# Kernel tuning notes

Measured on AMD Instinct MI355X. Metric: run time of the kernel, lower is better.

Reference implementation:

```python
import jax, jax.numpy as jnp
import numpy as np

H = 3        # num heads
K_ = 16      # codebook size per head (k_**H == k == 4096)
D = 768      # full vector dim
DH = D // H  # per-head dim


def setup_inputs() -> dict:
    key = jax.random.key(0)
    kx, kk, ka = jax.random.split(key, 3)
    x = jax.random.normal(kx, (16, 4096, D), dtype=jnp.float32)
    kernel = jax.random.normal(kk, (H, K_, DH), dtype=jnp.float32)
    alpha = jax.random.uniform(ka, (), dtype=jnp.float32)
    return {"x": x, "kernel": kernel, "alpha": alpha}


def reference(x, kernel, alpha):
    B, S, _ = x.shape
    xh = x.reshape(B, S, H, DH)  # split into per-head chunks
    # squared L2 distance [B,S,H,K_]; argmin identical to argmin of tf.norm
    sq = (jnp.sum(xh * xh, axis=-1)[..., None]
          - 2.0 * jnp.einsum('bshd,hkd->bshk', xh, kernel)
          + jnp.sum(kernel * kernel, axis=-1))
    ind = jnp.argmin(sq, axis=-1)              # [B,S,H] int
    v = kernel[jnp.arange(H), ind]             # per-head gather -> [B,S,H,DH]
    v = v.reshape(B, S, D)
    out = alpha * x + (1.0 - alpha) * v        # convex blend
    base = (K_ ** jnp.arange(H)).astype(ind.dtype)  # [1, K_, K_^2]
    code = jnp.sum(ind * base, axis=-1)        # packed code [B,S]
    return out, code
```

## Files before the change

### kernel.cpp

```cpp
#include <hip/hip_runtime.h>


#define NH 3
#define NK 16
#define DHEAD 256
#define DFULL 768
#define TB 4

typedef float f2 __attribute__((ext_vector_type(2)));

__device__ __forceinline__ float dpp_xor1(float x) {
    return __builtin_bit_cast(float, __builtin_amdgcn_mov_dpp(
        __builtin_bit_cast(int, x), 0xB1, 0xF, 0xF, false));
}
__device__ __forceinline__ float dpp_xor2(float x) {
    return __builtin_bit_cast(float, __builtin_amdgcn_mov_dpp(
        __builtin_bit_cast(int, x), 0x4E, 0xF, 0xF, false));
}
__device__ __forceinline__ float swz_xor4(float x) {
    return __builtin_bit_cast(float, __builtin_amdgcn_ds_swizzle(
        __builtin_bit_cast(int, x), 0x101F));
}
__device__ __forceinline__ float swz_xor8(float x) {
    return __builtin_bit_cast(float, __builtin_amdgcn_ds_swizzle(
        __builtin_bit_cast(int, x), 0x201F));
}
__device__ __forceinline__ float swz_xor16(float x) {
    return __builtin_bit_cast(float, __builtin_amdgcn_ds_swizzle(
        __builtin_bit_cast(int, x), 0x401F));
}

__global__ __launch_bounds__(256, 4) void rvq_head_kernel(
    const float* __restrict__ x,
    const float* __restrict__ cb,
    const float* __restrict__ alphap,
    float* __restrict__ out,
    float* __restrict__ codef,
    int tok_per_block)
{
    const int h = blockIdx.y;
    __shared__ float lc[NK * DHEAD];
    __shared__ float lps[NK * 16];
    __shared__ float lcn[NK];

    const int tid = threadIdx.x;

    const float4* cb4 = (const float4*)(cb + (size_t)h * NK * DHEAD);
    float4* lc4w = (float4*)lc;
    #pragma unroll
    for (int i = 0; i < 4; ++i) lc4w[tid + i * 256] = cb4[tid + i * 256];

    {
        const int r = tid >> 4, dd = (tid & 15) * 16;
        const float4* p = (const float4*)(cb + (size_t)h * NK * DHEAD + r * DHEAD + dd);
        float s = 0.f;
        #pragma unroll
        for (int q = 0; q < 4; ++q) {
            float4 c = p[q];
            s += c.x * c.x + c.y * c.y + c.z * c.z + c.w * c.w;
        }
        lps[tid] = s;
    }
    __syncthreads();
    if (tid < NK) {
        float s = 0.f;
        #pragma unroll
        for (int q = 0; q < 16; ++q) s += lps[tid * 16 + q];
        lcn[tid] = s;
    }
    __syncthreads();

    const int lane = tid & 63;
    const int wid  = tid >> 6;
    const int hl = (((lane >> 1) & 1) << 3) | ((lane & 1) << 2)
                 | (((lane >> 2) & 1) << 1) | ((lane >> 3) & 1);
    const float cn_l  = lcn[hl];
    const float alpha = alphap[0];
    const float beta  = 1.0f - alpha;
    const float kscale = (float)(1 << (4 * h));

    const float4* x4   = (const float4*)x;
    float4* out4       = (float4*)out;
    const float4* lc4  = (const float4*)lc;

    const int t_base = blockIdx.x * tok_per_block;
    const int t_end  = t_base + tok_per_block;

    for (int t0 = t_base + wid * TB; t0 < t_end; t0 += 4 * TB) {
        float4 xf[TB];
        #pragma unroll
        for (int t = 0; t < TB; ++t)
            xf[t] = x4[(size_t)(t0 + t) * (DFULL / 4) + h * 64 + lane];

        float v[TB][NK];
        #pragma unroll
        for (int j = 0; j < NK; ++j) {
            float4 c = lc4[((j ^ hl) << 6) | lane];
            #pragma unroll
            for (int t = 0; t < TB; ++t) {
                f2 p = (f2){xf[t].x, xf[t].y} * (f2){c.x, c.y};
                p += (f2){xf[t].z, xf[t].w} * (f2){c.z, c.w};
                v[t][j] = p.x + p.y;
            }
        }

        #pragma unroll
        for (int t = 0; t < TB; ++t) {
            #pragma unroll
            for (int j = 0; j < 8; ++j) v[t][j] += dpp_xor2(v[t][j + 8]);
            #pragma unroll
            for (int j = 0; j < 4; ++j) v[t][j] += dpp_xor1(v[t][j + 4]);
            #pragma unroll
            for (int j = 0; j < 2; ++j) v[t][j] += swz_xor4(v[t][j + 2]);
            v[t][0] += swz_xor8(v[t][1]);
            v[t][0] += swz_xor16(v[t][0]);
            v[t][0] += __shfl_xor(v[t][0], 32);
        }

        #pragma unroll
        for (int t = 0; t < TB; ++t) {
            const float sc = cn_l - 2.0f * v[t][0];
            float m = sc;
            m = fminf(m, dpp_xor1(m));
            m = fminf(m, dpp_xor2(m));
            m = fminf(m, swz_xor4(m));
            m = fminf(m, swz_xor8(m));
            const unsigned long long mask = __ballot(sc == m);
            const int lmin = __builtin_ctzll(mask);
            const int bi = (((lmin >> 1) & 1) << 3) | ((lmin & 1) << 2)
                         | (((lmin >> 2) & 1) << 1) | ((lmin >> 3) & 1);
            const float4 c = lc4[(bi << 6) | lane];
            float4 o;
            o.x = alpha * xf[t].x + beta * c.x;
            o.y = alpha * xf[t].y + beta * c.y;
            o.z = alpha * xf[t].z + beta * c.z;
            o.w = alpha * xf[t].w + beta * c.w;
            out4[(size_t)(t0 + t) * (DFULL / 4) + h * 64 + lane] = o;
            if (lane == 0) atomicAdd(codef + t0 + t, (float)bi * kscale);
        }
    }
}

extern "C" void kernel_launch(void* const* d_in, const int* in_sizes, int n_in,
                              void* d_out, int out_size, void* d_ws, size_t ws_size,
                              hipStream_t stream) {
    const float* x      = (const float*)d_in[0];
    const float* cb     = (const float*)d_in[1];
    const float* alphap = (const float*)d_in[2];
    const int n_tokens  = in_sizes[0] / DFULL;
    float* out   = (float*)d_out;
    float* codef = out + (size_t)n_tokens * DFULL;

    hipMemsetAsync(codef, 0, (size_t)n_tokens * sizeof(float), stream);

    const int grid_x = 512;
    const int tok_per_block = n_tokens / grid_x;
    dim3 grid(grid_x, NH);
    rvq_head_kernel<<<grid, 256, 0, stream>>>(x, cb, alphap, out, codef,
                                              tok_per_block);
}
```

Baseline: 358.6 us.

## Prefetch next token batch, batch code atomics, enlarge blocks and grid

Software-pipelines the x loads: each wave issues the global loads for its next group of tokens before computing distances on the current group, and issues the first load before the codebook staging into shared memory. The four per-token code atomics are merged into a single atomic instruction with one lane per token. Blocks grow to 512 threads with a higher occupancy hint and the grid doubles in x. The aim is to hide global-memory latency in a bandwidth-bound kernel, at the cost of more registers for the prefetch buffers and fewer tokens per block.

```diff
diff --git a/kernel.cpp b/kernel.cpp
--- a/kernel.cpp
+++ b/kernel.cpp
@@ -6,6 +6,8 @@
 #define DHEAD 256
 #define DFULL 768
 #define TB 4
+#define BLK 512
+#define NWAVE (BLK / 64)
 
 typedef float f2 __attribute__((ext_vector_type(2)));
 
@@ -30,7 +32,7 @@
         __builtin_bit_cast(int, x), 0x401F));
 }
 
-__global__ __launch_bounds__(256, 4) void rvq_head_kernel(
+__global__ __launch_bounds__(BLK, 6) void rvq_head_kernel(
     const float* __restrict__ x,
     const float* __restrict__ cb,
     const float* __restrict__ alphap,
@@ -40,17 +42,32 @@
 {
     const int h = blockIdx.y;
     __shared__ float lc[NK * DHEAD];
-    __shared__ float lps[NK * 16];
+    __shared__ float lps[256];
     __shared__ float lcn[NK];
 
-    const int tid = threadIdx.x;
+    const int tid  = threadIdx.x;
+    const int lane = tid & 63;
+    const int wid  = tid >> 6;
+
+    const int t_base = blockIdx.x * tok_per_block;
+    const int t_end  = t_base + tok_per_block;
+    const int step   = NWAVE * TB;
+
+    const float4* x4 = (const float4*)x;
+    float4* out4     = (float4*)out;
+
+    int t0 = t_base + wid * TB;
+    float4 xf[TB];
+    #pragma unroll
+    for (int t = 0; t < TB; ++t)
+        xf[t] = x4[(size_t)(t0 + t) * (DFULL / 4) + h * 64 + lane];
 
     const float4* cb4 = (const float4*)(cb + (size_t)h * NK * DHEAD);
     float4* lc4w = (float4*)lc;
     #pragma unroll
-    for (int i = 0; i < 4; ++i) lc4w[tid + i * 256] = cb4[tid + i * 256];
+    for (int i = 0; i < 2; ++i) lc4w[tid + i * BLK] = cb4[tid + i * BLK];
 
-    {
+    if (tid < 256) {
         const int r = tid >> 4, dd = (tid & 15) * 16;
         const float4* p = (const float4*)(cb + (size_t)h * NK * DHEAD + r * DHEAD + dd);
         float s = 0.f;
@@ -70,8 +87,6 @@
     }
     __syncthreads();
 
-    const int lane = tid & 63;
-    const int wid  = tid >> 6;
     const int hl = (((lane >> 1) & 1) << 3) | ((lane & 1) << 2)
                  | (((lane >> 2) & 1) << 1) | ((lane >> 3) & 1);
     const float cn_l  = lcn[hl];
@@ -79,18 +94,17 @@
     const float beta  = 1.0f - alpha;
     const float kscale = (float)(1 << (4 * h));
 
-    const float4* x4   = (const float4*)x;
-    float4* out4       = (float4*)out;
-    const float4* lc4  = (const float4*)lc;
+    const float4* lc4 = (const float4*)lc;
 
-    const int t_base = blockIdx.x * tok_per_block;
-    const int t_end  = t_base + tok_per_block;
+    while (t0 < t_end) {
+        const int t1 = t0 + step;
 
-    for (int t0 = t_base + wid * TB; t0 < t_end; t0 += 4 * TB) {
-        float4 xf[TB];
-        #pragma unroll
-        for (int t = 0; t < TB; ++t)
-            xf[t] = x4[(size_t)(t0 + t) * (DFULL / 4) + h * 64 + lane];
+        float4 xn[TB];
+        if (t1 < t_end) {
+            #pragma unroll
+            for (int t = 0; t < TB; ++t)
+                xn[t] = x4[(size_t)(t1 + t) * (DFULL / 4) + h * 64 + lane];
+        }
 
         float v[TB][NK];
         #pragma unroll
@@ -117,6 +131,7 @@
             v[t][0] += __shfl_xor(v[t][0], 32);
         }
 
+        float bif[TB];
         #pragma unroll
         for (int t = 0; t < TB; ++t) {
             const float sc = cn_l - 2.0f * v[t][0];
@@ -136,8 +151,16 @@
             o.z = alpha * xf[t].z + beta * c.z;
             o.w = alpha * xf[t].w + beta * c.w;
             out4[(size_t)(t0 + t) * (DFULL / 4) + h * 64 + lane] = o;
-            if (lane == 0) atomicAdd(codef + t0 + t, (float)bi * kscale);
+            bif[t] = (float)bi * kscale;
         }
+
+        const float mya = (lane == 0) ? bif[0] : (lane == 1) ? bif[1]
+                        : (lane == 2) ? bif[2] : bif[3];
+        if (lane < TB) atomicAdd(codef + t0 + lane, mya);
+
+        t0 = t1;
+        #pragma unroll
+        for (int t = 0; t < TB; ++t) xf[t] = xn[t];
     }
 }
 
@@ -153,9 +176,9 @@
 
     hipMemsetAsync(codef, 0, (size_t)n_tokens * sizeof(float), stream);
 
-    const int grid_x = 512;
+    const int grid_x = 1024;
     const int tok_per_block = n_tokens / grid_x;
     dim3 grid(grid_x, NH);
-    rvq_head_kernel<<<grid, 256, 0, stream>>>(x, cb, alphap, out, codef,
+    rvq_head_kernel<<<grid, BLK, 0, stream>>>(x, cb, alphap, out, codef,
                                               tok_per_block);
 }
```

Measured after the change: 693.9 us. +93.5%, slower.
